# Performance work log

Measured on AMD Instinct MI355X. Metric: run time of the kernel, lower is better.

Reference implementation:

```python
import jax, jax.numpy as jnp
import numpy as np

N, F_IN, F_OUT, HEADS = 4096, 128, 64, 4


def setup_inputs() -> dict:
    key = jax.random.key(0)
    k1, k2, k3, k4, k5 = jax.random.split(key, 5)
    X = jax.random.normal(k1, (N, F_IN), dtype=jnp.float32)
    A = jax.random.randint(k2, (N, N), 0, 2, dtype=jnp.int32)
    # zero the diagonal: the torch loop always prepends the self node, so the
    # adjacency must not also contain it (would duplicate the self term).
    A = A * (1 - jnp.eye(N, dtype=jnp.int32))
    # per-head Linear(F_IN, F_OUT) weights/bias and Linear(2*F_OUT, 1, bias=False)
    W = jax.random.normal(k3, (HEADS, F_OUT, F_IN), dtype=jnp.float32) / np.sqrt(F_IN)
    b = jax.random.normal(k4, (HEADS, F_OUT), dtype=jnp.float32) * 0.02
    att = jax.random.normal(k5, (HEADS, 2 * F_OUT), dtype=jnp.float32) / np.sqrt(2 * F_OUT)
    return {"X": X, "A": A, "W": W, "b": b, "att": att}


def reference(X, A, W, b, att):
    # H[h, n, o] = line_h(X)
    H = jnp.einsum('nf,hof->hno', X, W) + b[:, None, :]
    f_out = W.shape[1]
    a_src, a_dst = att[:, :f_out], att[:, f_out:]
    # score e_ij = leaky_relu(a_src.H_i + a_dst.H_j)
    s = jnp.einsum('hno,ho->hn', H, a_src)  # query-side term (xi_bar expanded)
    d = jnp.einsum('hno,ho->hn', H, a_dst)  # neighbor-side term
    e = jax.nn.leaky_relu(s[:, :, None] + d[:, None, :])  # [H, N, N]
    # neighbor set = {self} U {j : A_ij != 0}
    mask = (A > 0) | jnp.eye(A.shape[0], dtype=bool)
    e = jnp.where(mask[None], e, -jnp.inf)
    alpha = jax.nn.softmax(e, axis=-1)  # segment softmax per node row
    # weighted sum per head, then mean over heads (sum / head in the original)
    out = jnp.einsum('hnm,hmo->no', alpha, H) / W.shape[0]
    return out  # [N, F_OUT]
```

## Files before the change

kernel.cpp:

```cpp
#include <hip/hip_runtime.h>
#include <hip/hip_bf16.h>


#define NN 4096
#define FIN 128
#define FOUT 64
#define NH 4

typedef __attribute__((ext_vector_type(8))) short bf16x8;
typedef __attribute__((ext_vector_type(4))) float f32x4;
typedef __attribute__((ext_vector_type(4))) unsigned int u32x4;

__device__ __forceinline__ unsigned short f32_bf16(float f) {
    unsigned u = __builtin_bit_cast(unsigned, f);
    u += 0x7fffu + ((u >> 16) & 1u);
    return (unsigned short)(u >> 16);
}

__global__ __launch_bounds__(256) void pack_bits(
    const int* __restrict__ A, unsigned long long* __restrict__ Abits)
{
    const int row  = blockIdx.x;
    const int lane = threadIdx.x & 63;
    const int wv   = threadIdx.x >> 6;
    const int* arow = A + (size_t)row * NN;
    #pragma unroll 4
    for (int c = 0; c < 16; ++c) {
        const int col = c * 256 + wv * 64 + lane;
        unsigned long long m = __ballot(__builtin_nontemporal_load(&arow[col]) > 0);
        if (lane == 0) Abits[(size_t)row * 64 + c * 4 + wv] = m;
    }
}

__global__ __launch_bounds__(256) void gat_prep(
    const float* __restrict__ X, const float* __restrict__ W,
    const float* __restrict__ b, const float* __restrict__ att,
    unsigned short* __restrict__ HbfT, float* __restrict__ Hrow,
    float* __restrict__ s_out, float* __restrict__ d_out,
    float* __restrict__ es_g, float* __restrict__ es2_g,
    float* __restrict__ ed_g, float* __restrict__ ed2_g)
{
    const int rb = blockIdx.x;
    const int h  = blockIdx.y;
    const int n0 = rb * 32;
    const int t  = threadIdx.x;

    __shared__ float Xl[32][132];
    __shared__ float Wt[128][68];

    for (int g = t; g < 32 * 32; g += 256) {
        int row = g >> 5, c4 = g & 31;
        float4 v = *(const float4*)&X[(size_t)(n0 + row) * FIN + c4 * 4];
        *(float4*)&Xl[row][c4 * 4] = v;
    }
    for (int g = t; g < 64 * 32; g += 256) {
        int o = g >> 5, c4 = g & 31;
        float4 v = *(const float4*)&W[((size_t)h * FOUT + o) * FIN + c4 * 4];
        Wt[c4 * 4 + 0][o] = v.x; Wt[c4 * 4 + 1][o] = v.y;
        Wt[c4 * 4 + 2][o] = v.z; Wt[c4 * 4 + 3][o] = v.w;
    }
    __syncthreads();

    const int rg = t >> 4;
    const int og = t & 15;
    float acc[2][4] = {};

    #pragma unroll 4
    for (int f4 = 0; f4 < 32; ++f4) {
        float xv[2][4], wv[4][4];
        #pragma unroll
        for (int i = 0; i < 2; ++i) {
            float4 tmp = *(const float4*)&Xl[rg * 2 + i][f4 * 4];
            xv[i][0] = tmp.x; xv[i][1] = tmp.y; xv[i][2] = tmp.z; xv[i][3] = tmp.w;
        }
        #pragma unroll
        for (int k = 0; k < 4; ++k) {
            float4 tmp = *(const float4*)&Wt[f4 * 4 + k][og * 4];
            wv[k][0] = tmp.x; wv[k][1] = tmp.y; wv[k][2] = tmp.z; wv[k][3] = tmp.w;
        }
        #pragma unroll
        for (int i = 0; i < 2; ++i)
            #pragma unroll
            for (int k = 0; k < 4; ++k)
                #pragma unroll
                for (int jj = 0; jj < 4; ++jj)
                    acc[i][jj] = fmaf(xv[i][k], wv[k][jj], acc[i][jj]);
    }

    float bb[4], as_[4], ad_[4];
    #pragma unroll
    for (int jj = 0; jj < 4; ++jj) {
        bb[jj]  = b[h * FOUT + og * 4 + jj];
        as_[jj] = att[h * 2 * FOUT + og * 4 + jj];
        ad_[jj] = att[h * 2 * FOUT + FOUT + og * 4 + jj];
    }
    #pragma unroll
    for (int i = 0; i < 2; ++i)
        #pragma unroll
        for (int jj = 0; jj < 4; ++jj)
            acc[i][jj] += bb[jj];

    float sp[2] = {0.f, 0.f}, dp[2] = {0.f, 0.f};
    #pragma unroll
    for (int i = 0; i < 2; ++i)
        #pragma unroll
        for (int jj = 0; jj < 4; ++jj) {
            sp[i] = fmaf(acc[i][jj], as_[jj], sp[i]);
            dp[i] = fmaf(acc[i][jj], ad_[jj], dp[i]);
        }
    #pragma unroll
    for (int off = 1; off < 16; off <<= 1) {
        #pragma unroll
        for (int i = 0; i < 2; ++i) {
            sp[i] += __shfl_xor(sp[i], off);
            dp[i] += __shfl_xor(dp[i], off);
        }
    }
    if (og == 0) {
        #pragma unroll
        for (int i = 0; i < 2; ++i) {
            int nn = n0 + rg * 2 + i;
            s_out[h * NN + nn]  = sp[i];
            d_out[h * NN + nn]  = dp[i];
            es_g [h * NN + nn]  = __expf(sp[i]);
            es2_g[h * NN + nn]  = __expf(0.01f * sp[i]);
            ed_g [h * NN + nn]  = __expf(dp[i]);
            ed2_g[h * NN + nn]  = __expf(0.01f * dp[i]);
        }
    }

    #pragma unroll
    for (int i = 0; i < 2; ++i) {
        float4 v = make_float4(acc[i][0], acc[i][1], acc[i][2], acc[i][3]);
        *(float4*)&Hrow[((size_t)h * NN + n0 + rg * 2 + i) * FOUT + og * 4] = v;
    }
    #pragma unroll
    for (int jj = 0; jj < 4; ++jj) {
        int o = og * 4 + jj;
        ushort2 p;
        p.x = f32_bf16(acc[0][jj]);
        p.y = f32_bf16(acc[1][jj]);
        *(ushort2*)&HbfT[((size_t)h * FOUT + o) * NN + n0 + rg * 2] = p;
    }
}

struct SMem {
    union {
        __align__(16) unsigned short H[2][64][128];
        struct {
            float red[6][16][68];
            float redl[6][16];
        } fin;
    };
};

__global__ __launch_bounds__(512, 4) void gat_main(
    const unsigned* __restrict__ Abits, const unsigned short* __restrict__ HbfT,
    const float* __restrict__ s_g, const float* __restrict__ d_g,
    const float* __restrict__ es_g, const float* __restrict__ es2_g,
    const float* __restrict__ ed_g, const float* __restrict__ ed2_g,
    const float* __restrict__ Hrow, float* __restrict__ outH)
{
    const int id   = blockIdx.x;
    const int h    = id & 3;
    const int tile = id >> 2;
    const int n0   = tile * 32;
    const int tid  = threadIdx.x;
    const int w    = tid >> 6;
    const int lane = tid & 63;
    const int r    = lane & 15;
    const int q    = lane >> 4;
    const int qs   = q * 8;
    const int rg   = w & 1;
    const int kg   = w >> 1;

    __shared__ SMem sm;

    const int nrow = n0 + rg * 16 + r;
    const float es  = es_g [h * NN + nrow];
    const float es2 = es2_g[h * NN + nrow];

    const int mb = (kg * 4 + q) ^ r;

    const int so = tid >> 4;
    const int sc = tid & 15;
    const unsigned short* srcA = HbfT + ((size_t)(h * FOUT) + so)      * NN + sc * 8;
    const unsigned short* srcB = HbfT + ((size_t)(h * FOUT) + so + 32) * NN + sc * 8;
    const int offA = so * 128        + (sc ^ (so & 15)) * 8;
    const int offB = (so + 32) * 128 + (sc ^ (so & 15)) * 8;

    const unsigned* bitsPtr = Abits + (size_t)nrow * 128 + kg;

    const float* edh  = ed_g  + h * NN + kg * 32 + qs;
    const float* ed2h = ed2_g + h * NN + kg * 32 + qs;

    bf16x8 ones;
    #pragma unroll
    for (int i = 0; i < 8; ++i) ones[i] = (short)0x3F80;

    f32x4 acc0 = {0,0,0,0}, acc1 = {0,0,0,0}, acc2 = {0,0,0,0},
          acc3 = {0,0,0,0}, accl = {0,0,0,0};

    bf16x8 stA, stB;

    stA = *(const bf16x8*)&srcA[0];
    stB = *(const bf16x8*)&srcB[0];
    float4 e0c = *(const float4*)&edh [0];
    float4 e1c = *(const float4*)&edh [4];
    float4 g0c = *(const float4*)&ed2h[0];
    float4 g1c = *(const float4*)&ed2h[4];
    unsigned bitsCur = bitsPtr[0];
    {
        unsigned short* hw = &sm.H[0][0][0];
        *(bf16x8*)(hw + offA) = stA;
        *(bf16x8*)(hw + offB) = stB;
    }
    __syncthreads();

    for (int ch = 0; ch < 32; ++ch) {
        const int buf = ch & 1;
        const unsigned short* hb = buf ? &sm.H[1][0][0] : &sm.H[0][0][0];

        float4 e0n, e1n, g0n, g1n;
        unsigned bitsNxt = 0;
        if (ch < 31) {
            stA = *(const bf16x8*)&srcA[(ch + 1) * 128];
            stB = *(const bf16x8*)&srcB[(ch + 1) * 128];
            e0n = *(const float4*)&edh [(ch + 1) * 128];
            e1n = *(const float4*)&edh [(ch + 1) * 128 + 4];
            g0n = *(const float4*)&ed2h[(ch + 1) * 128];
            g1n = *(const float4*)&ed2h[(ch + 1) * 128 + 4];
            bitsNxt = bitsPtr[(ch + 1) * 4];
        }

        const unsigned bits8 = bitsCur >> qs;
        const float edv [8] = {e0c.x, e0c.y, e0c.z, e0c.w, e1c.x, e1c.y, e1c.z, e1c.w};
        const float ed2v[8] = {g0c.x, g0c.y, g0c.z, g0c.w, g1c.x, g1c.y, g1c.z, g1c.w};

        u32x4 afu;
        #pragma unroll
        for (int p = 0; p < 4; ++p) {
            const int j0 = 2 * p, j1 = 2 * p + 1;
            float wa = (bits8 & (1u << j0))
                     ? fmaxf(es * edv[j0], es2 * ed2v[j0]) : 0.0f;
            float wb = (bits8 & (1u << j1))
                     ? fmaxf(es * edv[j1], es2 * ed2v[j1]) : 0.0f;
            __hip_bfloat162 pk = __float22bfloat162_rn(make_float2(wa, wb));
            unsigned u;
            __builtin_memcpy(&u, &pk, sizeof(u));
            afu[p] = u;
        }
        const bf16x8 af = __builtin_bit_cast(bf16x8, afu);

        const bf16x8 b0 = *(const bf16x8*)&hb[(r     ) * 128 + mb * 8];
        const bf16x8 b1 = *(const bf16x8*)&hb[(r + 16) * 128 + mb * 8];
        const bf16x8 b2 = *(const bf16x8*)&hb[(r + 32) * 128 + mb * 8];
        const bf16x8 b3 = *(const bf16x8*)&hb[(r + 48) * 128 + mb * 8];

        acc0 = __builtin_amdgcn_mfma_f32_16x16x32_bf16(af, b0,   acc0, 0, 0, 0);
        acc1 = __builtin_amdgcn_mfma_f32_16x16x32_bf16(af, b1,   acc1, 0, 0, 0);
        acc2 = __builtin_amdgcn_mfma_f32_16x16x32_bf16(af, b2,   acc2, 0, 0, 0);
        acc3 = __builtin_amdgcn_mfma_f32_16x16x32_bf16(af, b3,   acc3, 0, 0, 0);
        accl = __builtin_amdgcn_mfma_f32_16x16x32_bf16(af, ones, accl, 0, 0, 0);

        if (ch < 31) {
            unsigned short* hw = buf ? &sm.H[0][0][0] : &sm.H[1][0][0];
            *(bf16x8*)(hw + offA) = stA;
            *(bf16x8*)(hw + offB) = stB;
            e0c = e0n; e1c = e1n; g0c = g0n; g1c = g1n; bitsCur = bitsNxt;
        }
        __syncthreads();
    }

    if (kg > 0) {
        const int widx = (kg - 1) * 2 + rg;
        #pragma unroll
        for (int reg = 0; reg < 4; ++reg) {
            const int rr = q * 4 + reg;
            sm.fin.red[widx][rr][ 0 + r] = acc0[reg];
            sm.fin.red[widx][rr][16 + r] = acc1[reg];
            sm.fin.red[widx][rr][32 + r] = acc2[reg];
            sm.fin.red[widx][rr][48 + r] = acc3[reg];
        }
        if (r == 0) {
            #pragma unroll
            for (int reg = 0; reg < 4; ++reg)
                sm.fin.redl[widx][q * 4 + reg] = accl[reg];
        }
    }
    __syncthreads();
    if (kg == 0) {
        #pragma unroll
        for (int kk = 0; kk < 3; ++kk) {
            const int widx = kk * 2 + rg;
            #pragma unroll
            for (int reg = 0; reg < 4; ++reg) {
                const int rr = q * 4 + reg;
                acc0[reg] += sm.fin.red[widx][rr][ 0 + r];
                acc1[reg] += sm.fin.red[widx][rr][16 + r];
                acc2[reg] += sm.fin.red[widx][rr][32 + r];
                acc3[reg] += sm.fin.red[widx][rr][48 + r];
                accl[reg] += sm.fin.redl[widx][rr];
            }
        }
        #pragma unroll
        for (int reg = 0; reg < 4; ++reg) {
            const int rr  = q * 4 + reg;
            const int nn2 = n0 + rg * 16 + rr;
            const float tt = s_g[h * NN + nn2] + d_g[h * NN + nn2];
            const float wd = __expf(fmaxf(tt, 0.01f * tt));
            const float inv = 0.25f / (accl[reg] + wd);
            const float* hr = &Hrow[((size_t)h * NN + nn2) * FOUT];
            float*       ob = &outH[((size_t)h * NN + nn2) * FOUT];
            ob[ 0 + r] = (acc0[reg] + wd * hr[ 0 + r]) * inv;
            ob[16 + r] = (acc1[reg] + wd * hr[16 + r]) * inv;
            ob[32 + r] = (acc2[reg] + wd * hr[32 + r]) * inv;
            ob[48 + r] = (acc3[reg] + wd * hr[48 + r]) * inv;
        }
    }
}

__global__ __launch_bounds__(256) void gat_fin(
    const float* __restrict__ outH, float* __restrict__ out)
{
    const int i = blockIdx.x * 256 + threadIdx.x;
    const f32x4* p = (const f32x4*)outH;
    f32x4 v0 = __builtin_nontemporal_load(p + i);
    f32x4 v1 = __builtin_nontemporal_load(p + i +  65536);
    f32x4 v2 = __builtin_nontemporal_load(p + i + 131072);
    f32x4 v3 = __builtin_nontemporal_load(p + i + 196608);
    f32x4 s = (v0 + v1) + (v2 + v3);
    *((f32x4*)out + i) = s;
}

extern "C" void kernel_launch(void* const* d_in, const int* in_sizes, int n_in,
                              void* d_out, int out_size, void* d_ws, size_t ws_size,
                              hipStream_t stream) {
    const float* X   = (const float*)d_in[0];
    const int*   A   = (const int*)  d_in[1];
    const float* W   = (const float*)d_in[2];
    const float* b   = (const float*)d_in[3];
    const float* att = (const float*)d_in[4];
    float* out = (float*)d_out;

    char* ws = (char*)d_ws;
    unsigned short* HbfT = (unsigned short*)ws;
    size_t off = (size_t)NH * FOUT * NN * 2;
    float* s_buf   = (float*)(ws + off);  off += (size_t)NH * NN * 4;
    float* d_buf   = (float*)(ws + off);  off += (size_t)NH * NN * 4;
    float* es_buf  = (float*)(ws + off);  off += (size_t)NH * NN * 4;
    float* es2_buf = (float*)(ws + off);  off += (size_t)NH * NN * 4;
    float* ed_buf  = (float*)(ws + off);  off += (size_t)NH * NN * 4;
    float* ed2_buf = (float*)(ws + off);  off += (size_t)NH * NN * 4;
    unsigned long long* Abits = (unsigned long long*)(ws + off);
    off += (size_t)NN * 64 * 8;
    float* Hrow   = (float*)(ws + off);
    off += (size_t)NH * NN * FOUT * 4;
    float* outH   = (float*)(ws + off);
    off += (size_t)NH * NN * FOUT * 4;

    pack_bits<<<NN, 256, 0, stream>>>(A, Abits);
    gat_prep<<<dim3(128, 4), 256, 0, stream>>>(X, W, b, att, HbfT, Hrow,
                                               s_buf, d_buf,
                                               es_buf, es2_buf, ed_buf, ed2_buf);
    gat_main<<<512, 512, 0, stream>>>((const unsigned*)Abits, HbfT,
                                      s_buf, d_buf,
                                      es_buf, es2_buf, ed_buf, ed2_buf,
                                      Hrow, outH);
    gat_fin<<<256, 256, 0, stream>>>(outH, out);
}
```

Before: 172.7 us.

## Double K-chunk size to 256 and stage adjacency bits and ed vectors in LDS

The main aggregation loop now processes 256 neighbor columns per iteration (16 iterations instead of 32), so the number of block-wide barriers is halved. Adjacency bit words and the ed/ed2 vectors are loaded cooperatively into double-buffered shared memory instead of being fetched redundantly by every wave. Each iteration issues two MFMA groups. The cost is a larger LDS footprint, which may limit the four-blocks-per-CU occupancy target, and higher register pressure from the extra prefetch registers.

```diff
diff --git a/kernel.cpp b/kernel.cpp
--- a/kernel.cpp
+++ b/kernel.cpp
@@ -146,12 +146,15 @@
 
 struct SMem {
     union {
-        __align__(16) unsigned short H[2][64][128];
+        __align__(16) unsigned short H[2][64][256];
         struct {
             float red[6][16][68];
             float redl[6][16];
         } fin;
     };
+    unsigned bits[2][32][9];
+    float ed [2][256];
+    float ed2[2][256];
 };
 
 __global__ __launch_bounds__(512, 4) void gat_main(
@@ -180,19 +183,22 @@
     const float es  = es_g [h * NN + nrow];
     const float es2 = es2_g[h * NN + nrow];
 
-    const int mb = (kg * 4 + q) ^ r;
+    const int bb = ((kg * 4 + q) ^ r) & 15;
 
     const int so = tid >> 4;
     const int sc = tid & 15;
-    const unsigned short* srcA = HbfT + ((size_t)(h * FOUT) + so)      * NN + sc * 8;
-    const unsigned short* srcB = HbfT + ((size_t)(h * FOUT) + so + 32) * NN + sc * 8;
-    const int offA = so * 128        + (sc ^ (so & 15)) * 8;
-    const int offB = (so + 32) * 128 + (sc ^ (so & 15)) * 8;
-
-    const unsigned* bitsPtr = Abits + (size_t)nrow * 128 + kg;
-
-    const float* edh  = ed_g  + h * NN + kg * 32 + qs;
-    const float* ed2h = ed2_g + h * NN + kg * 32 + qs;
+    const unsigned short* baseA = HbfT + ((size_t)(h * FOUT) + so)      * NN + sc * 8;
+    const unsigned short* baseB = HbfT + ((size_t)(h * FOUT) + so + 32) * NN + sc * 8;
+    const int offA0 = so * 256        + ((sc ^ so) & 15) * 8;
+    const int offA1 = offA0 + 128;
+    const int offB0 = (so + 32) * 256 + ((sc ^ so) & 15) * 8;
+    const int offB1 = offB0 + 128;
+    const int brow = tid >> 3, bwd = tid & 7;
+    const unsigned* bitsSrc = Abits + (size_t)(n0 + brow) * 128 + bwd;
+    const int ei = tid & 63;
+    const float* edSrc  = ((tid < 320) ? ed_g : ed2_g) + (size_t)h * NN + ei * 4;
+    float* edDst0 = (tid < 320) ? sm.ed[0] : sm.ed2[0];
+    float* edDst1 = (tid < 320) ? sm.ed[1] : sm.ed2[1];
 
     bf16x8 ones;
     #pragma unroll
@@ -201,73 +207,123 @@
     f32x4 acc0 = {0,0,0,0}, acc1 = {0,0,0,0}, acc2 = {0,0,0,0},
           acc3 = {0,0,0,0}, accl = {0,0,0,0};
 
-    bf16x8 stA, stB;
-
-    stA = *(const bf16x8*)&srcA[0];
-    stB = *(const bf16x8*)&srcB[0];
-    float4 e0c = *(const float4*)&edh [0];
-    float4 e1c = *(const float4*)&edh [4];
-    float4 g0c = *(const float4*)&ed2h[0];
-    float4 g1c = *(const float4*)&ed2h[4];
-    unsigned bitsCur = bitsPtr[0];
     {
+        bf16x8 sA0 = *(const bf16x8*)&baseA[0];
+        bf16x8 sA1 = *(const bf16x8*)&baseA[128];
+        bf16x8 sB0 = *(const bf16x8*)&baseB[0];
+        bf16x8 sB1 = *(const bf16x8*)&baseB[128];
         unsigned short* hw = &sm.H[0][0][0];
-        *(bf16x8*)(hw + offA) = stA;
-        *(bf16x8*)(hw + offB) = stB;
+        *(bf16x8*)&hw[offA0] = sA0;
+        *(bf16x8*)&hw[offA1] = sA1;
+        *(bf16x8*)&hw[offB0] = sB0;
+        *(bf16x8*)&hw[offB1] = sB1;
+        if (tid < 256)      sm.bits[0][brow][bwd] = bitsSrc[0];
+        else if (tid < 384) *(float4*)&edDst0[ei * 4] = *(const float4*)&edSrc[0];
     }
     __syncthreads();
 
-    for (int ch = 0; ch < 32; ++ch) {
+    #pragma unroll 2
+    for (int ch = 0; ch < 16; ++ch) {
         const int buf = ch & 1;
         const unsigned short* hb = buf ? &sm.H[1][0][0] : &sm.H[0][0][0];
-
-        float4 e0n, e1n, g0n, g1n;
-        unsigned bitsNxt = 0;
-        if (ch < 31) {
-            stA = *(const bf16x8*)&srcA[(ch + 1) * 128];
-            stB = *(const bf16x8*)&srcB[(ch + 1) * 128];
-            e0n = *(const float4*)&edh [(ch + 1) * 128];
-            e1n = *(const float4*)&edh [(ch + 1) * 128 + 4];
-            g0n = *(const float4*)&ed2h[(ch + 1) * 128];
-            g1n = *(const float4*)&ed2h[(ch + 1) * 128 + 4];
-            bitsNxt = bitsPtr[(ch + 1) * 4];
-        }
-
-        const unsigned bits8 = bitsCur >> qs;
-        const float edv [8] = {e0c.x, e0c.y, e0c.z, e0c.w, e1c.x, e1c.y, e1c.z, e1c.w};
-        const float ed2v[8] = {g0c.x, g0c.y, g0c.z, g0c.w, g1c.x, g1c.y, g1c.z, g1c.w};
-
-        u32x4 afu;
-        #pragma unroll
-        for (int p = 0; p < 4; ++p) {
-            const int j0 = 2 * p, j1 = 2 * p + 1;
-            float wa = (bits8 & (1u << j0))
-                     ? fmaxf(es * edv[j0], es2 * ed2v[j0]) : 0.0f;
-            float wb = (bits8 & (1u << j1))
-                     ? fmaxf(es * edv[j1], es2 * ed2v[j1]) : 0.0f;
-            __hip_bfloat162 pk = __float22bfloat162_rn(make_float2(wa, wb));
-            unsigned u;
-            __builtin_memcpy(&u, &pk, sizeof(u));
-            afu[p] = u;
-        }
-        const bf16x8 af = __builtin_bit_cast(bf16x8, afu);
-
-        const bf16x8 b0 = *(const bf16x8*)&hb[(r     ) * 128 + mb * 8];
-        const bf16x8 b1 = *(const bf16x8*)&hb[(r + 16) * 128 + mb * 8];
-        const bf16x8 b2 = *(const bf16x8*)&hb[(r + 32) * 128 + mb * 8];
-        const bf16x8 b3 = *(const bf16x8*)&hb[(r + 48) * 128 + mb * 8];
-
-        acc0 = __builtin_amdgcn_mfma_f32_16x16x32_bf16(af, b0,   acc0, 0, 0, 0);
-        acc1 = __builtin_amdgcn_mfma_f32_16x16x32_bf16(af, b1,   acc1, 0, 0, 0);
-        acc2 = __builtin_amdgcn_mfma_f32_16x16x32_bf16(af, b2,   acc2, 0, 0, 0);
-        acc3 = __builtin_amdgcn_mfma_f32_16x16x32_bf16(af, b3,   acc3, 0, 0, 0);
-        accl = __builtin_amdgcn_mfma_f32_16x16x32_bf16(af, ones, accl, 0, 0, 0);
-
-        if (ch < 31) {
+        const unsigned (*bl)[9]  = buf ? sm.bits[1]     : sm.bits[0];
+        const float* edl         = buf ? sm.ed[1]       : sm.ed[0];
+        const float* ed2l        = buf ? sm.ed2[1]      : sm.ed2[0];
+
+        bf16x8 sA0, sA1, sB0, sB1; unsigned stBits = 0; float4 stEd;
+        if (ch < 15) {
+            const int c0n = (ch + 1) * 256;
+            sA0 = *(const bf16x8*)&baseA[c0n];
+            sA1 = *(const bf16x8*)&baseA[c0n + 128];
+            sB0 = *(const bf16x8*)&baseB[c0n];
+            sB1 = *(const bf16x8*)&baseB[c0n + 128];
+            if (tid < 256)      stBits = bitsSrc[(ch + 1) * 8];
+            else if (tid < 384) stEd = *(const float4*)&edSrc[c0n];
+        }
+
+        {
+            const unsigned bits8 = bl[rg * 16 + r][kg] >> qs;
+            const float4 e0 = *(const float4*)&edl [kg * 32 + qs];
+            const float4 e1 = *(const float4*)&edl [kg * 32 + qs + 4];
+            const float4 g0 = *(const float4*)&ed2l[kg * 32 + qs];
+            const float4 g1 = *(const float4*)&ed2l[kg * 32 + qs + 4];
+            const float edv [8] = {e0.x, e0.y, e0.z, e0.w, e1.x, e1.y, e1.z, e1.w};
+            const float ed2v[8] = {g0.x, g0.y, g0.z, g0.w, g1.x, g1.y, g1.z, g1.w};
+            u32x4 afu;
+            #pragma unroll
+            for (int p = 0; p < 4; ++p) {
+                const int j0 = 2 * p, j1 = 2 * p + 1;
+                float wa = (bits8 & (1u << j0))
+                         ? fmaxf(es * edv[j0], es2 * ed2v[j0]) : 0.0f;
+                float wb = (bits8 & (1u << j1))
+                         ? fmaxf(es * edv[j1], es2 * ed2v[j1]) : 0.0f;
+                __hip_bfloat162 pk = __float22bfloat162_rn(make_float2(wa, wb));
+                unsigned u;
+                __builtin_memcpy(&u, &pk, sizeof(u));
+                afu[p] = u;
+            }
+            const bf16x8 af = __builtin_bit_cast(bf16x8, afu);
+
+            const bf16x8 b0 = *(const bf16x8*)&hb[(r     ) * 256 + bb * 8];
+            const bf16x8 b1 = *(const bf16x8*)&hb[(r + 16) * 256 + bb * 8];
+            const bf16x8 b2 = *(const bf16x8*)&hb[(r + 32) * 256 + bb * 8];
+            const bf16x8 b3 = *(const bf16x8*)&hb[(r + 48) * 256 + bb * 8];
+
+            acc0 = __builtin_amdgcn_mfma_f32_16x16x32_bf16(af, b0,   acc0, 0, 0, 0);
+            acc1 = __builtin_amdgcn_mfma_f32_16x16x32_bf16(af, b1,   acc1, 0, 0, 0);
+            acc2 = __builtin_amdgcn_mfma_f32_16x16x32_bf16(af, b2,   acc2, 0, 0, 0);
+            acc3 = __builtin_amdgcn_mfma_f32_16x16x32_bf16(af, b3,   acc3, 0, 0, 0);
+            accl = __builtin_amdgcn_mfma_f32_16x16x32_bf16(af, ones, accl, 0, 0, 0);
+        }
+
+        {
+            const unsigned bits8 = bl[rg * 16 + r][kg + 4] >> qs;
+            const float4 e0 = *(const float4*)&edl [128 + kg * 32 + qs];
+            const float4 e1 = *(const float4*)&edl [128 + kg * 32 + qs + 4];
+            const float4 g0 = *(const float4*)&ed2l[128 + kg * 32 + qs];
+            const float4 g1 = *(const float4*)&ed2l[128 + kg * 32 + qs + 4];
+            const float edv [8] = {e0.x, e0.y, e0.z, e0.w, e1.x, e1.y, e1.z, e1.w};
+            const float ed2v[8] = {g0.x, g0.y, g0.z, g0.w, g1.x, g1.y, g1.z, g1.w};
+            u32x4 afu;
+            #pragma unroll
+            for (int p = 0; p < 4; ++p) {
+                const int j0 = 2 * p, j1 = 2 * p + 1;
+                float wa = (bits8 & (1u << j0))
+                         ? fmaxf(es * edv[j0], es2 * ed2v[j0]) : 0.0f;
+                float wb = (bits8 & (1u << j1))
+                         ? fmaxf(es * edv[j1], es2 * ed2v[j1]) : 0.0f;
+                __hip_bfloat162 pk = __float22bfloat162_rn(make_float2(wa, wb));
+                unsigned u;
+                __builtin_memcpy(&u, &pk, sizeof(u));
+                afu[p] = u;
+            }
+            const bf16x8 af = __builtin_bit_cast(bf16x8, afu);
+
+            const bf16x8 b0 = *(const bf16x8*)&hb[(r     ) * 256 + 128 + bb * 8];
+            const bf16x8 b1 = *(const bf16x8*)&hb[(r + 16) * 256 + 128 + bb * 8];
+            const bf16x8 b2 = *(const bf16x8*)&hb[(r + 32) * 256 + 128 + bb * 8];
+            const bf16x8 b3 = *(const bf16x8*)&hb[(r + 48) * 256 + 128 + bb * 8];
+
+            acc0 = __builtin_amdgcn_mfma_f32_16x16x32_bf16(af, b0,   acc0, 0, 0, 0);
+            acc1 = __builtin_amdgcn_mfma_f32_16x16x32_bf16(af, b1,   acc1, 0, 0, 0);
+            acc2 = __builtin_amdgcn_mfma_f32_16x16x32_bf16(af, b2,   acc2, 0, 0, 0);
+            acc3 = __builtin_amdgcn_mfma_f32_16x16x32_bf16(af, b3,   acc3, 0, 0, 0);
+            accl = __builtin_amdgcn_mfma_f32_16x16x32_bf16(af, ones, accl, 0, 0, 0);
+        }
+
+        if (ch < 15) {
             unsigned short* hw = buf ? &sm.H[0][0][0] : &sm.H[1][0][0];
-            *(bf16x8*)(hw + offA) = stA;
-            *(bf16x8*)(hw + offB) = stB;
-            e0c = e0n; e1c = e1n; g0c = g0n; g1c = g1n; bitsCur = bitsNxt;
+            *(bf16x8*)&hw[offA0] = sA0;
+            *(bf16x8*)&hw[offA1] = sA1;
+            *(bf16x8*)&hw[offB0] = sB0;
+            *(bf16x8*)&hw[offB1] = sB1;
+            if (tid < 256) {
+                unsigned* bw = buf ? &sm.bits[0][0][0] : &sm.bits[1][0][0];
+                bw[brow * 9 + bwd] = stBits;
+            } else if (tid < 384) {
+                float* ew = buf ? edDst0 : edDst1;
+                *(float4*)&ew[ei * 4] = stEd;
+            }
         }
         __syncthreads();
     }
```

Result: faster. 161.8 us (-6.3%).
